# Kernel optimization log

Hardware: AMD Instinct MI355X
Metric: run time of the kernel (lower is better)

Reference implementation:

```python
import jax, jax.numpy as jnp
import numpy as np

V = 1_000_000   # number of nodes in graph (embedding table rows)
D_IN = 128      # input feature dim
D_OUT = 384     # output dim (3 * D_OUT//3)
N_UNIQ = 20_000 # unique nodes in batch
K = 32          # neighbors per node (num_walks)
B = 40_000      # batch of node lookups


def setup_inputs() -> dict:
    key = jax.random.key(0)
    ks = jax.random.split(key, 12)
    d3 = D_OUT // 3
    return {
        "unique_nodes": jax.random.randint(ks[0], (N_UNIQ,), 0, V),
        "adj_neighbors": jax.random.randint(ks[1], (N_UNIQ, K), 0, V),
        "dis_neighbors": jax.random.randint(ks[2], (N_UNIQ, K), 0, V),
        "nodes_idx": jax.random.randint(ks[3], (B,), 0, N_UNIQ),
        "feat_table": jax.random.normal(ks[4], (V, D_IN), dtype=jnp.float32),
        # linear weights stored [in, out] (transposed vs torch nn.Linear)
        "W_self": jax.random.uniform(ks[5], (D_IN, d3), minval=-0.1, maxval=0.1, dtype=jnp.float32),
        "W_adj": jax.random.uniform(ks[6], (D_IN, d3), minval=-0.1, maxval=0.1, dtype=jnp.float32),
        "W_dis": jax.random.uniform(ks[7], (D_IN, d3), minval=-0.1, maxval=0.1, dtype=jnp.float32),
        "bias": jnp.zeros((D_OUT,), dtype=jnp.float32),
        "WC_w": jax.random.normal(ks[8], (D_OUT, D_OUT), dtype=jnp.float32) * 0.05,
        "WC_b": jnp.zeros((D_OUT,), dtype=jnp.float32),
    }


def reference(unique_nodes, adj_neighbors, dis_neighbors, nodes_idx,
              feat_table, W_self, W_adj, W_dis, bias, WC_w, WC_b):
    # MeanAggregator: one-hot mask.mm(embed) == mean of gathered neighbor feats
    adj_agg = jnp.mean(feat_table[adj_neighbors], axis=1)   # [N,K,D] -> [N,D]
    dis_agg = jnp.mean(feat_table[dis_neighbors], axis=1)
    self_feats = feat_table[unique_nodes] @ W_self           # [N, D_OUT/3]
    adj_feats = adj_agg @ W_adj
    dis_feats = dis_agg @ W_dis
    # concat + bias, WC linear, leakyReLU(0.2), L2-normalize (eval mode: no dropout)
    feats = jnp.concatenate([self_feats, adj_feats, dis_feats], axis=-1) + bias
    feats = feats @ WC_w + WC_b
    feats = jnp.where(feats >= 0, feats, 0.2 * feats)
    norm = jnp.maximum(jnp.linalg.norm(feats, axis=-1, keepdims=True), 1e-12)
    feats = feats / norm
    return feats[nodes_idx]  # [B, D_OUT]
```

## Files before the change

kernel.cpp:

```cpp
#include <hip/hip_runtime.h>
#include <hip/hip_bf16.h>

#define N_UNIQ 20000
#define K_NBR 32
#define BATCH 40000

typedef unsigned short ushort_t;
typedef __bf16 bfrag __attribute__((ext_vector_type(8)));
typedef float  ffrag __attribute__((ext_vector_type(4)));
typedef unsigned uvec4 __attribute__((ext_vector_type(4)));

__device__ __forceinline__ ushort_t f2bf(float f) {
    unsigned u = __builtin_bit_cast(unsigned, f);
    unsigned r = u + 0x7fffu + ((u >> 16) & 1u);
    return (ushort_t)(r >> 16);
}
__device__ __forceinline__ unsigned pack2(float x, float y) {
    return (unsigned)f2bf(x) | ((unsigned)f2bf(y) << 16);
}

__global__ void pack_agg_kernel(const float* __restrict__ Ws,
                                const float* __restrict__ Wa,
                                const float* __restrict__ Wd,
                                const float* __restrict__ WC,
                                uint4* __restrict__ wp1,
                                uint4* __restrict__ wp2,
                                const int* __restrict__ uniq,
                                const int* __restrict__ adjn,
                                const int* __restrict__ disn,
                                const float* __restrict__ feat,
                                ushort_t* __restrict__ F) {
    if (blockIdx.x < 96) {
        int t = blockIdx.x * blockDim.x + threadIdx.x;
        int l = t & 63, q = l >> 4, m = l & 15;
        ushort_t v[8];
        if (t < 6144) {
            int g   = t >> 11;
            int rem = t & 2047;
            int nt  = rem >> 8;
            int kk  = (rem >> 6) & 3;
            const float* W = (g == 0) ? Ws : ((g == 1) ? Wa : Wd);
#pragma unroll
            for (int j = 0; j < 8; j++)
                v[j] = f2bf(W[(kk * 32 + q * 8 + j) * 128 + nt * 16 + m]);
            uint4 u; __builtin_memcpy(&u, v, 16);
            wp1[t] = u;
        } else {
            int t2 = t - 6144;
            int nt = t2 / 768;
            int kk = (t2 >> 6) % 12;
#pragma unroll
            for (int j = 0; j < 8; j++)
                v[j] = f2bf(WC[(kk * 32 + q * 8 + j) * 384 + nt * 16 + m]);
            uint4 u; __builtin_memcpy(&u, v, 16);
            wp2[t2] = u;
        }
        return;
    }

    int node = ((blockIdx.x - 96) << 2) + (threadIdx.x >> 6);
    node = __builtin_amdgcn_readfirstlane(node);
    if (node >= N_UNIQ) return;

    const int l   = threadIdx.x & 63;
    const int lm  = l & 31;
    const bool isdis = (l >= 32);

    const int* __restrict__ na = adjn + node * K_NBR;
    const int* __restrict__ nd = disn + node * K_NBR;
    const float4* __restrict__ feat4 = (const float4*)feat;

    float ax = 0.f, ay = 0.f, az = 0.f, aw = 0.f;
#pragma unroll
    for (int i = 0; i < K_NBR; i++) {
        int ra = na[i];
        int rd = nd[i];
        int r  = isdis ? rd : ra;
        int idx = r * 32 + lm;
        float4 v = feat4[idx];
        ax += v.x; ay += v.y; az += v.z; aw += v.w;
    }

    const float inv = 1.0f / 32.0f;
    ushort_t* row = F + (size_t)node * 384;

    uint2 mpk;
    mpk.x = pack2(ax * inv, ay * inv);
    mpk.y = pack2(az * inv, aw * inv);
    *(uint2*)(row + 128 + (isdis ? 128 : 0) + lm * 4) = mpk;

    if (!isdis) {
        int rs = uniq[node];
        float4 sv = feat4[rs * 32 + lm];
        uint2 spk;
        spk.x = pack2(sv.x, sv.y);
        spk.y = pack2(sv.z, sv.w);
        *(uint2*)(row + lm * 4) = spk;
    }
}

__global__ void gemm1_kernel(ushort_t* __restrict__ F,
                             const uint4* __restrict__ wp1,
                             const float* __restrict__ bias) {
    int grp = blockIdx.x;
    int w   = threadIdx.x >> 6;
    int l = threadIdx.x & 63, q = l >> 4, m = l & 15;
    int m0 = grp * 16;

    uint4 a[12];
    const ushort_t* xrow = F + (size_t)(m0 + m) * 384;
#pragma unroll
    for (int kk = 0; kk < 12; kk++)
        a[kk] = *(const uint4*)(xrow + kk * 32 + q * 8);

    ushort_t outv[6][4];
    int nts[6];
#pragma unroll
    for (int n = 0; n < 6; n++) {
        const int g = n >> 1;
        int nt = g * 8 + w * 2 + (n & 1);
        nts[n] = nt;
        ffrag acc = {0.f, 0.f, 0.f, 0.f};
        const uint4* wp = wp1 + (size_t)nt * 4 * 64;
#pragma unroll
        for (int kk = 0; kk < 4; kk++) {
            bfrag bf = __builtin_bit_cast(bfrag, wp[kk * 64 + l]);
            bfrag af = __builtin_bit_cast(bfrag, a[g * 4 + kk]);
            acc = __builtin_amdgcn_mfma_f32_16x16x32_bf16(af, bf, acc, 0, 0, 0);
        }
        float bv = bias[nt * 16 + m];
#pragma unroll
        for (int r = 0; r < 4; r++) outv[n][r] = f2bf(acc[r] + bv);
    }
    __syncthreads();
#pragma unroll
    for (int n = 0; n < 6; n++) {
        int col = nts[n] * 16 + m;
#pragma unroll
        for (int r = 0; r < 4; r++)
            F[(size_t)(m0 + q * 4 + r) * 384 + col] = outv[n][r];
    }
}

__global__ void gemm2_kernel(const ushort_t* __restrict__ F,
                             const uint4* __restrict__ wp2,
                             const float* __restrict__ wcb,
                             float* __restrict__ G) {
    __shared__ float ssred[4][16];
    int grp = blockIdx.x;
    int w   = threadIdx.x >> 6;
    int nt0 = w * 6;
    int l = threadIdx.x & 63, q = l >> 4, m = l & 15;
    int m0 = grp * 16;

    uint4 a[12];
    const ushort_t* xrow = F + (size_t)(m0 + m) * 384;
#pragma unroll
    for (int kk = 0; kk < 12; kk++)
        a[kk] = *(const uint4*)(xrow + kk * 32 + q * 8);

    float vals[6][4];
    float ss[4] = {0.f, 0.f, 0.f, 0.f};
#pragma unroll
    for (int n = 0; n < 6; n++) {
        int nt = nt0 + n;
        ffrag acc = {0.f, 0.f, 0.f, 0.f};
        const uint4* wp = wp2 + (size_t)nt * 12 * 64;
#pragma unroll
        for (int kk = 0; kk < 12; kk++) {
            bfrag bf = __builtin_bit_cast(bfrag, wp[kk * 64 + l]);
            bfrag af = __builtin_bit_cast(bfrag, a[kk]);
            acc = __builtin_amdgcn_mfma_f32_16x16x32_bf16(af, bf, acc, 0, 0, 0);
        }
        float bv = wcb[nt * 16 + m];
#pragma unroll
        for (int r = 0; r < 4; r++) {
            float v = acc[r] + bv;
            v = (v >= 0.f) ? v : 0.2f * v;
            vals[n][r] = v;
            ss[r] += v * v;
        }
    }
#pragma unroll
    for (int r = 0; r < 4; r++) {
        float s = ss[r];
        s += __shfl_xor(s, 1);
        s += __shfl_xor(s, 2);
        s += __shfl_xor(s, 4);
        s += __shfl_xor(s, 8);
        ss[r] = s;
    }
    if (m == 0) {
#pragma unroll
        for (int r = 0; r < 4; r++) ssred[w][q * 4 + r] = ss[r];
    }
    __syncthreads();

    float invn[4];
#pragma unroll
    for (int r = 0; r < 4; r++) {
        int row = q * 4 + r;
        float tot = ssred[0][row] + ssred[1][row] + ssred[2][row] + ssred[3][row];
        invn[r] = 1.0f / fmaxf(sqrtf(tot), 1e-12f);
    }
#pragma unroll
    for (int n = 0; n < 6; n++) {
        int col = (nt0 + n) * 16 + m;
#pragma unroll
        for (int r = 0; r < 4; r++)
            G[(size_t)(m0 + q * 4 + r) * 384 + col] = vals[n][r] * invn[r];
    }
}

__global__ void gather_kernel(const int* __restrict__ nidx,
                              const uvec4* __restrict__ G4,
                              uvec4* __restrict__ out4) {
    int t = blockIdx.x * blockDim.x + threadIdx.x;
    if (t >= BATCH * 96) return;
    int b = t / 96, c = t - b * 96;
    int row = nidx[b];
    uvec4 v = G4[(size_t)row * 96 + c];
    __builtin_nontemporal_store(v, &out4[(size_t)b * 96 + c]);
}

extern "C" void kernel_launch(void* const* d_in, const int* in_sizes, int n_in,
                              void* d_out, int out_size, void* d_ws, size_t ws_size,
                              hipStream_t stream) {
    const int*   uniq = (const int*)d_in[0];
    const int*   adjn = (const int*)d_in[1];
    const int*   disn = (const int*)d_in[2];
    const int*   nidx = (const int*)d_in[3];
    const float* feat = (const float*)d_in[4];
    const float* Ws   = (const float*)d_in[5];
    const float* Wa   = (const float*)d_in[6];
    const float* Wd   = (const float*)d_in[7];
    const float* bias = (const float*)d_in[8];
    const float* WC   = (const float*)d_in[9];
    const float* wcb  = (const float*)d_in[10];

    ushort_t* F   = (ushort_t*)d_ws;
    float*    G   = (float*)((char*)d_ws + 15360000);
    uint4*    wp1 = (uint4*)((char*)d_ws + 46080000);
    uint4*    wp2 = (uint4*)((char*)d_ws + 46178304);

    pack_agg_kernel<<<96 + N_UNIQ / 4, 256, 0, stream>>>(
        Ws, Wa, Wd, WC, wp1, wp2, uniq, adjn, disn, feat, F);
    gemm1_kernel<<<N_UNIQ / 16, 256, 0, stream>>>(F, wp1, bias);
    gemm2_kernel<<<N_UNIQ / 16, 256, 0, stream>>>(F, wp2, wcb, G);
    gather_kernel<<<BATCH * 96 / 256, 256, 0, stream>>>(nidx, (const uvec4*)G, (uvec4*)d_out);
}
```

Before: 744.4 us.

## Pre-convert full feature table to bf16 before neighbor aggregation gather

Adds a pass that streams the whole 1M x 128 fp32 feature table and writes it as bf16 to workspace, then gathers neighbors from the bf16 copy so each random access reads half the bytes. The conversion reads 512 MB and writes 256 MB on every call, far more than the roughly 170 MB of random gathers it is meant to cheapen. It also rounds features to bf16 before averaging, which changes accuracy slightly. The new path runs only if the workspace is large enough.

```diff
diff --git a/kernel.cpp b/kernel.cpp
--- a/kernel.cpp
+++ b/kernel.cpp
@@ -9,6 +9,7 @@
 typedef __bf16 bfrag __attribute__((ext_vector_type(8)));
 typedef float  ffrag __attribute__((ext_vector_type(4)));
 typedef unsigned uvec4 __attribute__((ext_vector_type(4)));
+typedef unsigned uvec2 __attribute__((ext_vector_type(2)));
 
 __device__ __forceinline__ ushort_t f2bf(float f) {
     unsigned u = __builtin_bit_cast(unsigned, f);
@@ -17,6 +18,105 @@
 }
 __device__ __forceinline__ unsigned pack2(float x, float y) {
     return (unsigned)f2bf(x) | ((unsigned)f2bf(y) << 16);
+}
+__device__ __forceinline__ unsigned bfpack_bits(unsigned ux, unsigned uy) {
+    unsigned rx = ux + 0x7fffu + ((ux >> 16) & 1u);
+    unsigned ry = uy + 0x7fffu + ((uy >> 16) & 1u);
+    return (rx >> 16) | (ry & 0xffff0000u);
+}
+__device__ __forceinline__ float bf2f(unsigned hi16) {
+    return __builtin_bit_cast(float, hi16 << 16);
+}
+
+__global__ void conv_pack_kernel(const float* __restrict__ Ws,
+                                 const float* __restrict__ Wa,
+                                 const float* __restrict__ Wd,
+                                 const float* __restrict__ WC,
+                                 uint4* __restrict__ wp1,
+                                 uint4* __restrict__ wp2,
+                                 const float* __restrict__ feat,
+                                 uvec2* __restrict__ FB2) {
+    if (blockIdx.x < 96) {
+        int t = blockIdx.x * blockDim.x + threadIdx.x;
+        int l = t & 63, q = l >> 4, m = l & 15;
+        ushort_t v[8];
+        if (t < 6144) {
+            int g   = t >> 11;
+            int rem = t & 2047;
+            int nt  = rem >> 8;
+            int kk  = (rem >> 6) & 3;
+            const float* W = (g == 0) ? Ws : ((g == 1) ? Wa : Wd);
+#pragma unroll
+            for (int j = 0; j < 8; j++)
+                v[j] = f2bf(W[(kk * 32 + q * 8 + j) * 128 + nt * 16 + m]);
+            uint4 u; __builtin_memcpy(&u, v, 16);
+            wp1[t] = u;
+        } else {
+            int t2 = t - 6144;
+            int nt = t2 / 768;
+            int kk = (t2 >> 6) % 12;
+#pragma unroll
+            for (int j = 0; j < 8; j++)
+                v[j] = f2bf(WC[(kk * 32 + q * 8 + j) * 384 + nt * 16 + m]);
+            uint4 u; __builtin_memcpy(&u, v, 16);
+            wp2[t2] = u;
+        }
+        return;
+    }
+    const uvec4* __restrict__ f4 = (const uvec4*)feat;
+    const int total = 1000000 * 128 / 4;
+    int stride = (gridDim.x - 96) * blockDim.x;
+    for (int i = (blockIdx.x - 96) * blockDim.x + threadIdx.x; i < total; i += stride) {
+        uvec4 u = __builtin_nontemporal_load(&f4[i]);
+        uvec2 p;
+        p[0] = bfpack_bits(u[0], u[1]);
+        p[1] = bfpack_bits(u[2], u[3]);
+        FB2[i] = p;
+    }
+}
+
+__global__ void agg_bf16_kernel(const int* __restrict__ uniq,
+                                const int* __restrict__ adjn,
+                                const int* __restrict__ disn,
+                                const uvec2* __restrict__ FB2,
+                                ushort_t* __restrict__ F) {
+    int node = (blockIdx.x << 2) + (threadIdx.x >> 6);
+    node = __builtin_amdgcn_readfirstlane(node);
+    if (node >= N_UNIQ) return;
+
+    const int l   = threadIdx.x & 63;
+    const int lm  = l & 31;
+    const bool isdis = (l >= 32);
+
+    const int* __restrict__ na = adjn + node * K_NBR;
+    const int* __restrict__ nd = disn + node * K_NBR;
+
+    float ax = 0.f, ay = 0.f, az = 0.f, aw = 0.f;
+#pragma unroll
+    for (int i = 0; i < K_NBR; i++) {
+        int ra = na[i];
+        int rd = nd[i];
+        int r  = isdis ? rd : ra;
+        uvec2 v = FB2[r * 32 + lm];
+        ax += bf2f(v[0] & 0xffffu);
+        ay += bf2f(v[0] >> 16);
+        az += bf2f(v[1] & 0xffffu);
+        aw += bf2f(v[1] >> 16);
+    }
+
+    const float inv = 1.0f / 32.0f;
+    ushort_t* row = F + (size_t)node * 384;
+
+    uint2 mpk;
+    mpk.x = pack2(ax * inv, ay * inv);
+    mpk.y = pack2(az * inv, aw * inv);
+    *(uint2*)(row + 128 + (isdis ? 128 : 0) + lm * 4) = mpk;
+
+    if (!isdis) {
+        int rs = uniq[node];
+        uvec2 sv = FB2[rs * 32 + lm];
+        *(uvec2*)(row + lm * 4) = sv;
+    }
 }
 
 __global__ void pack_agg_kernel(const float* __restrict__ Ws,
@@ -242,9 +342,17 @@
     float*    G   = (float*)((char*)d_ws + 15360000);
     uint4*    wp1 = (uint4*)((char*)d_ws + 46080000);
     uint4*    wp2 = (uint4*)((char*)d_ws + 46178304);
-
-    pack_agg_kernel<<<96 + N_UNIQ / 4, 256, 0, stream>>>(
-        Ws, Wa, Wd, WC, wp1, wp2, uniq, adjn, disn, feat, F);
+    uvec2*    FB2 = (uvec2*)((char*)d_ws + 46473216);
+    const size_t NEED_A = 46473216ULL + 256000000ULL;
+
+    if (ws_size >= NEED_A) {
+        conv_pack_kernel<<<96 + 4096, 256, 0, stream>>>(
+            Ws, Wa, Wd, WC, wp1, wp2, feat, FB2);
+        agg_bf16_kernel<<<N_UNIQ / 4, 256, 0, stream>>>(uniq, adjn, disn, FB2, F);
+    } else {
+        pack_agg_kernel<<<96 + N_UNIQ / 4, 256, 0, stream>>>(
+            Ws, Wa, Wd, WC, wp1, wp2, uniq, adjn, disn, feat, F);
+    }
     gemm1_kernel<<<N_UNIQ / 16, 256, 0, stream>>>(F, wp1, bias);
     gemm2_kernel<<<N_UNIQ / 16, 256, 0, stream>>>(F, wp2, wcb, G);
     gather_kernel<<<BATCH * 96 / 256, 256, 0, stream>>>(nidx, (const uvec4*)G, (uvec4*)d_out);
```

Measured after the change: 818.2 us. 9.9% more time.
